# Optimization experiments

Measured on AMD Instinct MI355X. Metric: run time of the kernel, lower is better.

Reference implementation:

```python
import jax, jax.numpy as jnp
import numpy as np

N = 50000      # nodes
E = 200000     # edges
IN = 768       # in_dim
HID = 256      # hidden_dim
OUT = 64       # out_dim
H = 4          # heads in conv1
R = 6          # n_relations
NEG = 0.2      # LeakyReLU negative slope (PyG default)
EPS = 1e-5     # LayerNorm eps


def layer_norm(h, g, b):
    mu = jnp.mean(h, axis=-1, keepdims=True)
    var = jnp.mean((h - mu) ** 2, axis=-1, keepdims=True)
    return (h - mu) * jax.lax.rsqrt(var + EPS) * g + b


def gat_layer(x, src, dst, W, a_src, a_dst, bias, heads, dh):
    # project: [N, heads, dh]
    h = (x @ W).reshape(-1, heads, dh)
    # per-node attention logits [N, heads]
    al_s = jnp.sum(h * a_src, axis=-1)
    al_d = jnp.sum(h * a_dst, axis=-1)
    # per-edge scores (edge j->i: source contributes al_s[j], target al_d[i])
    e = jax.nn.leaky_relu(al_s[src] + al_d[dst], NEG)  # [E, heads]
    # segment softmax over edges sharing the same destination node
    e_max = jax.ops.segment_max(e, dst, num_segments=N)        # [N, heads]
    ex = jnp.exp(e - e_max[dst])                               # [E, heads]
    denom = jax.ops.segment_sum(ex, dst, num_segments=N)       # [N, heads]
    alpha = ex / denom[dst]                                    # [E, heads]
    # weighted scatter-aggregate of source messages
    msg = h[src] * alpha[:, :, None]                            # [E, heads, dh]
    out = jax.ops.segment_sum(msg, dst, num_segments=N)        # [N, heads, dh]
    return out.reshape(-1, heads * dh) + bias


def setup_inputs() -> dict:
    key = jax.random.key(0)
    ks = jax.random.split(key, 16)
    s = 0.05  # keep attention logits tame
    return {
        "x": jax.random.normal(ks[0], (N, IN), jnp.float32),
        "edge_index": jax.random.randint(ks[1], (2, E), 0, N, dtype=jnp.int64),
        "edge_type": jax.random.randint(ks[2], (E,), 0, R, dtype=jnp.int64),
        "edge_emb": jax.random.normal(ks[3], (R, IN), jnp.float32) * s,
        "W1": jax.random.normal(ks[4], (IN, H * (HID // H)), jnp.float32) * s,
        "a_src1": jax.random.normal(ks[5], (H, HID // H), jnp.float32) * s,
        "a_dst1": jax.random.normal(ks[6], (H, HID // H), jnp.float32) * s,
        "b1": jnp.zeros((HID,), jnp.float32),
        "g1": jnp.ones((HID,), jnp.float32),
        "be1": jnp.zeros((HID,), jnp.float32),
        "W2": jax.random.normal(ks[7], (HID, OUT), jnp.float32) * s,
        "a_src2": jax.random.normal(ks[8], (1, OUT), jnp.float32) * s,
        "a_dst2": jax.random.normal(ks[9], (1, OUT), jnp.float32) * s,
        "b2": jnp.zeros((OUT,), jnp.float32),
        "g2": jnp.ones((OUT,), jnp.float32),
        "be2": jnp.zeros((OUT,), jnp.float32),
    }


def reference(x, edge_index, edge_type, edge_emb, W1, a_src1, a_dst1, b1, g1, be1,
              W2, a_src2, a_dst2, b2, g2, be2):
    src, dst = edge_index[0], edge_index[1]
    edge_feat = edge_emb[edge_type]                 # [E, IN]
    x_mod = x.at[src].set(x[src] + edge_feat)
    h = gat_layer(x_mod, src, dst, W1, a_src1, a_dst1, b1, H, HID // H)
    h = layer_norm(h, g1, be1)
    h = jax.nn.elu(h)                                # dropout off (inference)
    h = gat_layer(h, src, dst, W2, a_src2, a_dst2, b2, 1, OUT)
    h = layer_norm(h, g2, be2)
    return h
```

## Files before the change

### kernel.cpp

```cpp
#include <hip/hip_runtime.h>
#include <cstdint>
#include <cstddef>

#define NN 50000
#define NE 200000
#define IND 768
#define HID 256
#define OUTD 64
#define NB 196

typedef __bf16 bf16;
typedef __bf16 bf16x8 __attribute__((ext_vector_type(8)));
typedef float f32x4 __attribute__((ext_vector_type(4)));

__global__ __launch_bounds__(256) void k_edge_prep(const int* __restrict__ ei,
                                                   int* __restrict__ le, int* __restrict__ deg) {
  int e = blockIdx.x * 256 + threadIdx.x;
  if (e < NE) {
    atomicMax(&le[ei[e]], e);
    atomicAdd(&deg[ei[NE + e]], 1);
  }
}

__global__ __launch_bounds__(256) void k_eembz(const float* __restrict__ eemb,
                                               float* __restrict__ ez) {
  int i = blockIdx.x * 256 + threadIdx.x;
  if (i < 7 * IND) ez[i] = (i < 6 * IND) ? eemb[i] : 0.f;
}

__global__ __launch_bounds__(256) void k_prep_a(const float* __restrict__ x,
                                                const int* __restrict__ le,
                                                const int* __restrict__ et,
                                                const float* __restrict__ eembz,
                                                bf16* __restrict__ A1) {
  int idx = blockIdx.x * 256 + threadIdx.x;
  if (idx >= NN * (IND / 8)) return;
  int row = idx / (IND / 8);
  int c = (idx - row * (IND / 8)) * 8;
  int l = le[row];
  int e = (l >= 0) ? et[l] : 6;
  const float* px = x + (size_t)row * IND + c;
  const float* pe = eembz + (size_t)e * IND + c;
  float4 v0 = *(const float4*)px, v1 = *(const float4*)(px + 4);
  float4 e0 = *(const float4*)pe, e1 = *(const float4*)(pe + 4);
  bf16x8 o;
  o[0] = (bf16)(v0.x + e0.x); o[1] = (bf16)(v0.y + e0.y);
  o[2] = (bf16)(v0.z + e0.z); o[3] = (bf16)(v0.w + e0.w);
  o[4] = (bf16)(v1.x + e1.x); o[5] = (bf16)(v1.y + e1.y);
  o[6] = (bf16)(v1.z + e1.z); o[7] = (bf16)(v1.w + e1.w);
  *(bf16x8*)(A1 + (size_t)row * IND + c) = o;
}

__global__ __launch_bounds__(256) void k_scan_block(const int* __restrict__ deg,
                                                    int* __restrict__ excl, int* __restrict__ bsum) {
  __shared__ int sm[256];
  int tid = threadIdx.x;
  int i = blockIdx.x * 256 + tid;
  int v = (i < NN) ? deg[i] : 0;
  sm[tid] = v;
  __syncthreads();
#pragma unroll
  for (int off = 1; off < 256; off <<= 1) {
    int t = (tid >= off) ? sm[tid - off] : 0;
    __syncthreads();
    sm[tid] += t;
    __syncthreads();
  }
  if (i < NN) excl[i] = sm[tid] - v;
  if (tid == 255) bsum[blockIdx.x] = sm[255];
}

__global__ __launch_bounds__(256) void k_scan_partials(const int* __restrict__ bsum,
                                                       int* __restrict__ bbase) {
  __shared__ int sm[256];
  int tid = threadIdx.x;
  int v = (tid < NB) ? bsum[tid] : 0;
  sm[tid] = v;
  __syncthreads();
#pragma unroll
  for (int off = 1; off < 256; off <<= 1) {
    int t = (tid >= off) ? sm[tid - off] : 0;
    __syncthreads();
    sm[tid] += t;
    __syncthreads();
  }
  bbase[tid] = sm[tid] - v;
}

__global__ __launch_bounds__(256) void k_add_base(const int* __restrict__ excl,
                                                  const int* __restrict__ bbase,
                                                  int* __restrict__ rowstart, int* __restrict__ cur) {
  int i = blockIdx.x * 256 + threadIdx.x;
  if (i < NN) {
    int rs = excl[i] + bbase[i >> 8];
    rowstart[i] = rs;
    cur[i] = rs;
  }
}

__global__ __launch_bounds__(256) void k_scatter_csr(const int* __restrict__ ei,
                                                     int* __restrict__ cur, int* __restrict__ csr) {
  int e = blockIdx.x * 256 + threadIdx.x;
  if (e < NE) {
    int d = ei[NE + e];
    int pos = atomicAdd(&cur[d], 1);
    csr[pos] = ei[e];
  }
}

__global__ __launch_bounds__(256) void k_transpose(const float* __restrict__ W,
                                                   bf16* __restrict__ Wt, int K, int NC) {
  int k = blockIdx.x * 256 + threadIdx.x;
  int n = blockIdx.y;
  if (k < K) Wt[n * K + k] = (bf16)W[k * NC + n];
}

__device__ __forceinline__ void gld16(const bf16* g, bf16* l) {
  __builtin_amdgcn_global_load_lds((const __attribute__((address_space(1))) void*)g,
                                   (__attribute__((address_space(3))) void*)l, 16, 0, 0);
}

template <typename OutT>
__global__ __launch_bounds__(256) void k_gemm_bt(const bf16* __restrict__ A,
                                                 const bf16* __restrict__ Bt,
                                                 OutT* __restrict__ C,
                                                 int M, int K, int NC,
                                                 const float* __restrict__ aS,
                                                 const float* __restrict__ aD,
                                                 float* __restrict__ alS,
                                                 float* __restrict__ alD,
                                                 int alStride) {
  __shared__ bf16 As[128 * 32];
  __shared__ bf16 Bs[128 * 32];
  const int tid = threadIdx.x;
  const int lane = tid & 63;
  const int wave = tid >> 6;
  const int wr = wave >> 1, wc = wave & 1;
  const int ln15 = lane & 15, q = lane >> 4;
  const int n0 = blockIdx.x * 128;
  const int m0 = blockIdx.y * 128;

  const int sr = lane >> 2;
  const int scol = (lane & 3) * 8;
  const int gA0 = min(m0 + wave * 32 + sr, M - 1);
  const int gA1 = min(m0 + wave * 32 + 16 + sr, M - 1);
  const int gB0 = min(n0 + wave * 32 + sr, NC - 1);
  const int gB1 = min(n0 + wave * 32 + 16 + sr, NC - 1);
  bf16* lA0 = As + (wave * 32) * 32;
  bf16* lA1 = As + (wave * 32 + 16) * 32;
  bf16* lB0 = Bs + (wave * 32) * 32;
  bf16* lB1 = Bs + (wave * 32 + 16) * 32;

  f32x4 acc[4][4] = {};

  for (int kt = 0; kt < K; kt += 32) {
    gld16(A + (size_t)gA0 * K + kt + scol, lA0);
    gld16(A + (size_t)gA1 * K + kt + scol, lA1);
    gld16(Bt + (size_t)gB0 * K + kt + scol, lB0);
    gld16(Bt + (size_t)gB1 * K + kt + scol, lB1);
    __syncthreads();
    bf16x8 af[4], bfr[4];
#pragma unroll
    for (int i = 0; i < 4; i++)
      af[i] = *(const bf16x8*)(As + (wr * 64 + i * 16 + ln15) * 32 + q * 8);
#pragma unroll
    for (int i = 0; i < 4; i++)
      bfr[i] = *(const bf16x8*)(Bs + (wc * 64 + i * 16 + ln15) * 32 + q * 8);
#pragma unroll
    for (int mi = 0; mi < 4; mi++)
#pragma unroll
      for (int ni = 0; ni < 4; ni++)
        acc[mi][ni] = __builtin_amdgcn_mfma_f32_16x16x32_bf16(af[mi], bfr[ni], acc[mi][ni], 0, 0, 0);
    __syncthreads();
  }

#pragma unroll
  for (int mi = 0; mi < 4; mi++)
#pragma unroll
    for (int ni = 0; ni < 4; ni++)
#pragma unroll
      for (int r = 0; r < 4; r++) {
        int row = m0 + wr * 64 + mi * 16 + q * 4 + r;
        int col = n0 + wc * 64 + ni * 16 + ln15;
        if (row < M && col < NC) C[(size_t)row * NC + col] = (OutT)acc[mi][ni][r];
      }

  if (n0 + wc * 64 < NC) {
    const int hd = (n0 + wc * 64) >> 6;
#pragma unroll
    for (int mi = 0; mi < 4; mi++)
#pragma unroll
      for (int r = 0; r < 4; r++) {
        float ps = 0.f, pd = 0.f;
#pragma unroll
        for (int ni = 0; ni < 4; ni++) {
          int col = n0 + wc * 64 + ni * 16 + ln15;
          float w_s = (col < NC) ? aS[col] : 0.f;
          float w_d = (col < NC) ? aD[col] : 0.f;
          ps += acc[mi][ni][r] * w_s;
          pd += acc[mi][ni][r] * w_d;
        }
#pragma unroll
        for (int off = 1; off < 16; off <<= 1) {
          ps += __shfl_xor(ps, off);
          pd += __shfl_xor(pd, off);
        }
        int row = m0 + wr * 64 + mi * 16 + q * 4 + r;
        if (ln15 == 0 && row < M) {
          alS[row * alStride + hd] = ps;
          alD[row * alStride + hd] = pd;
        }
      }
  }
}

__global__ __launch_bounds__(256) void k_agg_ln1(const int* __restrict__ rowstart,
                                                 const int* __restrict__ deg,
                                                 const int* __restrict__ csr,
                                                 const bf16* __restrict__ h1,
                                                 const float* __restrict__ alS,
                                                 const float* __restrict__ alD,
                                                 const float* __restrict__ b1,
                                                 const float* __restrict__ g1,
                                                 const float* __restrict__ be1,
                                                 bf16* __restrict__ hln) {
  __shared__ float red[8];
  int n = blockIdx.x, f = threadIdx.x, hd = f >> 6;
  int start = rowstart[n], cnt = deg[n];
  float ald = alD[n * 4 + hd];
  float accv = 0.f, accw = 0.f;
  for (int j = 0; j < cnt; j++) {
    int s = csr[start + j];
    float logit = alS[s * 4 + hd] + ald;
    logit = logit >= 0.f ? logit : 0.2f * logit;
    float w = __expf(logit);
    accv += w * (float)h1[(size_t)s * HID + f];
    accw += w;
  }
  float v = (cnt > 0) ? accv / accw : 0.f;
  v += b1[f];
  float s = v, ss = v * v;
#pragma unroll
  for (int off = 32; off; off >>= 1) { s += __shfl_xor(s, off); ss += __shfl_xor(ss, off); }
  if ((f & 63) == 0) { red[f >> 6] = s; red[4 + (f >> 6)] = ss; }
  __syncthreads();
  float tot = red[0] + red[1] + red[2] + red[3];
  float tss = red[4] + red[5] + red[6] + red[7];
  float mu = tot * (1.f / HID);
  float var = tss * (1.f / HID) - mu * mu;
  float y = (v - mu) * rsqrtf(var + 1e-5f) * g1[f] + be1[f];
  y = y > 0.f ? y : __expf(y) - 1.f;
  hln[(size_t)n * HID + f] = (bf16)y;
}

__global__ __launch_bounds__(64) void k_agg_ln2(const int* __restrict__ rowstart,
                                                const int* __restrict__ deg,
                                                const int* __restrict__ csr,
                                                const float* __restrict__ h2,
                                                const float* __restrict__ alS,
                                                const float* __restrict__ alD,
                                                const float* __restrict__ b2,
                                                const float* __restrict__ g2,
                                                const float* __restrict__ be2,
                                                float* __restrict__ out) {
  int n = blockIdx.x, f = threadIdx.x;
  int start = rowstart[n], cnt = deg[n];
  float ald = alD[n];
  float accv = 0.f, accw = 0.f;
  for (int j = 0; j < cnt; j++) {
    int s = csr[start + j];
    float logit = alS[s] + ald;
    logit = logit >= 0.f ? logit : 0.2f * logit;
    float w = __expf(logit);
    accv += w * h2[(size_t)s * OUTD + f];
    accw += w;
  }
  float v = (cnt > 0) ? accv / accw : 0.f;
  v += b2[f];
  float s = v, ss = v * v;
#pragma unroll
  for (int off = 32; off; off >>= 1) { s += __shfl_xor(s, off); ss += __shfl_xor(ss, off); }
  float mu = s * (1.f / OUTD);
  float var = ss * (1.f / OUTD) - mu * mu;
  out[(size_t)n * OUTD + f] = (v - mu) * rsqrtf(var + 1e-5f) * g2[f] + be2[f];
}

extern "C" void kernel_launch(void* const* d_in, const int* in_sizes, int n_in,
                              void* d_out, int out_size, void* d_ws, size_t ws_size,
                              hipStream_t stream) {
  const float* x    = (const float*)d_in[0];
  const int*   ei   = (const int*)d_in[1];
  const int*   et   = (const int*)d_in[2];
  const float* eemb = (const float*)d_in[3];
  const float* W1   = (const float*)d_in[4];
  const float* as1  = (const float*)d_in[5];
  const float* ad1  = (const float*)d_in[6];
  const float* b1   = (const float*)d_in[7];
  const float* g1   = (const float*)d_in[8];
  const float* be1  = (const float*)d_in[9];
  const float* W2   = (const float*)d_in[10];
  const float* as2  = (const float*)d_in[11];
  const float* ad2  = (const float*)d_in[12];
  const float* b2   = (const float*)d_in[13];
  const float* g2   = (const float*)d_in[14];
  const float* be2  = (const float*)d_in[15];
  float* out = (float*)d_out;

  char* base = (char*)d_ws;
  size_t off = 0;
  auto alloc = [&](size_t bytes) -> void* {
    void* p = base + off;
    off = (off + bytes + 255) & ~(size_t)255;
    return p;
  };
  int*   le    = (int*)alloc((size_t)NN * 4);
  int*   deg   = (int*)alloc((size_t)NN * 4);
  int*   excl  = (int*)alloc((size_t)NN * 4);
  int*   bsum  = (int*)alloc(256 * 4);
  int*   bbase = (int*)alloc(256 * 4);
  int*   rowst = (int*)alloc((size_t)NN * 4);
  int*   cur   = (int*)alloc((size_t)NN * 4);
  int*   csr   = (int*)alloc((size_t)NE * 4);
  bf16*  h1    = (bf16*)alloc((size_t)NN * HID * 2);
  float* alS1  = (float*)alloc((size_t)NN * 4 * 4);
  float* alD1  = (float*)alloc((size_t)NN * 4 * 4);
  bf16*  W1t   = (bf16*)alloc((size_t)HID * IND * 2);
  bf16*  W2t   = (bf16*)alloc((size_t)OUTD * HID * 2);
  float* eembz = (float*)alloc((size_t)7 * IND * 4);
  char*  R     = (char*)alloc((size_t)NN * IND * 2);
  bf16*  A1    = (bf16*)R;
  bf16*  hln   = (bf16*)R;
  float* h2    = (float*)(R + (size_t)NN * HID * 2);
  float* alS2  = (float*)(R + (size_t)NN * HID * 2 + (size_t)NN * OUTD * 4);
  float* alD2  = (float*)(R + (size_t)NN * HID * 2 + (size_t)NN * OUTD * 4 + (size_t)NN * 4);

  hipMemsetAsync(le, 0xFF, (size_t)NN * 4, stream);
  hipMemsetAsync(deg, 0, (size_t)NN * 4, stream);

  k_edge_prep<<<(NE + 255) / 256, 256, 0, stream>>>(ei, le, deg);
  k_eembz<<<(7 * IND + 255) / 256, 256, 0, stream>>>(eemb, eembz);
  k_prep_a<<<(NN * (IND / 8) + 255) / 256, 256, 0, stream>>>(x, le, et, eembz, A1);
  k_scan_block<<<NB, 256, 0, stream>>>(deg, excl, bsum);
  k_scan_partials<<<1, 256, 0, stream>>>(bsum, bbase);
  k_add_base<<<NB, 256, 0, stream>>>(excl, bbase, rowst, cur);
  k_scatter_csr<<<(NE + 255) / 256, 256, 0, stream>>>(ei, cur, csr);

  k_transpose<<<dim3(3, HID), 256, 0, stream>>>(W1, W1t, IND, HID);
  k_transpose<<<dim3(1, OUTD), 256, 0, stream>>>(W2, W2t, HID, OUTD);

  k_gemm_bt<bf16><<<dim3(2, (NN + 127) / 128), 256, 0, stream>>>(
      A1, W1t, h1, NN, IND, HID, as1, ad1, alS1, alD1, 4);
  k_agg_ln1<<<NN, 256, 0, stream>>>(rowst, deg, csr, h1, alS1, alD1, b1, g1, be1, hln);

  k_gemm_bt<float><<<dim3(1, (NN + 127) / 128), 256, 0, stream>>>(
      hln, W2t, h2, NN, HID, OUTD, as2, ad2, alS2, alD2, 1);
  k_agg_ln2<<<NN, 64, 0, stream>>>(rowst, deg, csr, h2, alS2, alD2, b2, g2, be2, out);
}
```

Measured before the change: 481.1 us.

## Double-buffer GEMM loads, add 64-wide tile variant, repack aggregation kernels per wave

The GEMM now double-buffers its LDS tiles and issues the next k-slice loads before computing on the current one, using explicit vmcnt waits. A template parameter adds a 64-column tile variant so the second GEMM no longer wastes half of a 128-wide tile. The layer-1 aggregation now processes one node per wave with 4 features per lane, using vectorized bf16 loads and a block-free LayerNorm reduction. Layer-2 aggregation packs 4 nodes into each 256-thread block. The hand-written waitcnt counts must match the number of issued global_load_lds calls, and they add complexity.

```diff
diff --git a/kernel.cpp b/kernel.cpp
--- a/kernel.cpp
+++ b/kernel.cpp
@@ -11,6 +11,7 @@
 
 typedef __bf16 bf16;
 typedef __bf16 bf16x8 __attribute__((ext_vector_type(8)));
+typedef __bf16 bf16x4 __attribute__((ext_vector_type(4)));
 typedef float f32x4 __attribute__((ext_vector_type(4)));
 
 __global__ __launch_bounds__(256) void k_edge_prep(const int* __restrict__ ei,
@@ -120,7 +121,7 @@
                                    (__attribute__((address_space(3))) void*)l, 16, 0, 0);
 }
 
-template <typename OutT>
+template <typename OutT, int TN>
 __global__ __launch_bounds__(256) void k_gemm_bt(const bf16* __restrict__ A,
                                                  const bf16* __restrict__ Bt,
                                                  OutT* __restrict__ C,
@@ -130,57 +131,88 @@
                                                  float* __restrict__ alS,
                                                  float* __restrict__ alD,
                                                  int alStride) {
-  __shared__ bf16 As[128 * 32];
-  __shared__ bf16 Bs[128 * 32];
+  constexpr int MI = (TN == 128) ? 4 : 2;
+  constexpr int WROWS = MI * 16;
+  __shared__ bf16 As[2][128 * 32];
+  __shared__ bf16 Bs[2][TN * 32];
   const int tid = threadIdx.x;
   const int lane = tid & 63;
   const int wave = tid >> 6;
-  const int wr = wave >> 1, wc = wave & 1;
+  const int wr = (TN == 128) ? (wave >> 1) : wave;
+  const int wc = (TN == 128) ? (wave & 1) : 0;
   const int ln15 = lane & 15, q = lane >> 4;
-  const int n0 = blockIdx.x * 128;
+  const int n0 = blockIdx.x * TN;
   const int m0 = blockIdx.y * 128;
 
   const int sr = lane >> 2;
   const int scol = (lane & 3) * 8;
   const int gA0 = min(m0 + wave * 32 + sr, M - 1);
   const int gA1 = min(m0 + wave * 32 + 16 + sr, M - 1);
-  const int gB0 = min(n0 + wave * 32 + sr, NC - 1);
-  const int gB1 = min(n0 + wave * 32 + 16 + sr, NC - 1);
-  bf16* lA0 = As + (wave * 32) * 32;
-  bf16* lA1 = As + (wave * 32 + 16) * 32;
-  bf16* lB0 = Bs + (wave * 32) * 32;
-  bf16* lB1 = Bs + (wave * 32 + 16) * 32;
-
-  f32x4 acc[4][4] = {};
-
-  for (int kt = 0; kt < K; kt += 32) {
-    gld16(A + (size_t)gA0 * K + kt + scol, lA0);
-    gld16(A + (size_t)gA1 * K + kt + scol, lA1);
-    gld16(Bt + (size_t)gB0 * K + kt + scol, lB0);
-    gld16(Bt + (size_t)gB1 * K + kt + scol, lB1);
-    __syncthreads();
-    bf16x8 af[4], bfr[4];
+  int gB0, gB1 = 0;
+  if constexpr (TN == 128) {
+    gB0 = min(n0 + wave * 32 + sr, NC - 1);
+    gB1 = min(n0 + wave * 32 + 16 + sr, NC - 1);
+  } else {
+    gB0 = min(n0 + wave * 16 + sr, NC - 1);
+  }
+
+  auto stage = [&](int buf, int kt) {
+    gld16(A + (size_t)gA0 * K + kt + scol, &As[buf][(wave * 32) * 32]);
+    gld16(A + (size_t)gA1 * K + kt + scol, &As[buf][(wave * 32 + 16) * 32]);
+    if constexpr (TN == 128) {
+      gld16(Bt + (size_t)gB0 * K + kt + scol, &Bs[buf][(wave * 32) * 32]);
+      gld16(Bt + (size_t)gB1 * K + kt + scol, &Bs[buf][(wave * 32 + 16) * 32]);
+    } else {
+      gld16(Bt + (size_t)gB0 * K + kt + scol, &Bs[buf][(wave * 16) * 32]);
+    }
+  };
+
+  f32x4 acc[MI][4] = {};
+
+  auto compute = [&](int buf) {
+    bf16x8 af[MI], bfr[4];
+#pragma unroll
+    for (int i = 0; i < MI; i++)
+      af[i] = *(const bf16x8*)(&As[buf][(wr * WROWS + i * 16 + ln15) * 32 + q * 8]);
 #pragma unroll
     for (int i = 0; i < 4; i++)
-      af[i] = *(const bf16x8*)(As + (wr * 64 + i * 16 + ln15) * 32 + q * 8);
-#pragma unroll
-    for (int i = 0; i < 4; i++)
-      bfr[i] = *(const bf16x8*)(Bs + (wc * 64 + i * 16 + ln15) * 32 + q * 8);
-#pragma unroll
-    for (int mi = 0; mi < 4; mi++)
+      bfr[i] = *(const bf16x8*)(&Bs[buf][(wc * 64 + i * 16 + ln15) * 32 + q * 8]);
+#pragma unroll
+    for (int mi = 0; mi < MI; mi++)
 #pragma unroll
       for (int ni = 0; ni < 4; ni++)
         acc[mi][ni] = __builtin_amdgcn_mfma_f32_16x16x32_bf16(af[mi], bfr[ni], acc[mi][ni], 0, 0, 0);
-    __syncthreads();
-  }
-
-#pragma unroll
-  for (int mi = 0; mi < 4; mi++)
+  };
+
+  const int NT = K >> 5;
+
+  stage(0, 0);
+  stage(1, 32);
+  int cur = 0;
+  for (int t = 0; t < NT; ++t) {
+    if (t < NT - 1) {
+      if constexpr (TN == 128) asm volatile("s_waitcnt vmcnt(4)" ::: "memory");
+      else                     asm volatile("s_waitcnt vmcnt(3)" ::: "memory");
+    } else {
+      asm volatile("s_waitcnt vmcnt(0)" ::: "memory");
+    }
+    __builtin_amdgcn_s_barrier();
+    compute(cur);
+    if (t + 2 < NT) {
+      asm volatile("s_waitcnt lgkmcnt(0)" ::: "memory");
+      __builtin_amdgcn_s_barrier();
+      stage(cur, (t + 2) << 5);
+    }
+    cur ^= 1;
+  }
+
+#pragma unroll
+  for (int mi = 0; mi < MI; mi++)
 #pragma unroll
     for (int ni = 0; ni < 4; ni++)
 #pragma unroll
       for (int r = 0; r < 4; r++) {
-        int row = m0 + wr * 64 + mi * 16 + q * 4 + r;
+        int row = m0 + wr * WROWS + mi * 16 + q * 4 + r;
         int col = n0 + wc * 64 + ni * 16 + ln15;
         if (row < M && col < NC) C[(size_t)row * NC + col] = (OutT)acc[mi][ni][r];
       }
@@ -188,7 +220,7 @@
   if (n0 + wc * 64 < NC) {
     const int hd = (n0 + wc * 64) >> 6;
 #pragma unroll
-    for (int mi = 0; mi < 4; mi++)
+    for (int mi = 0; mi < MI; mi++)
 #pragma unroll
       for (int r = 0; r < 4; r++) {
         float ps = 0.f, pd = 0.f;
@@ -205,7 +237,7 @@
           ps += __shfl_xor(ps, off);
           pd += __shfl_xor(pd, off);
         }
-        int row = m0 + wr * 64 + mi * 16 + q * 4 + r;
+        int row = m0 + wr * WROWS + mi * 16 + q * 4 + r;
         if (ln15 == 0 && row < M) {
           alS[row * alStride + hd] = ps;
           alD[row * alStride + hd] = pd;
@@ -224,46 +256,65 @@
                                                  const float* __restrict__ g1,
                                                  const float* __restrict__ be1,
                                                  bf16* __restrict__ hln) {
-  __shared__ float red[8];
-  int n = blockIdx.x, f = threadIdx.x, hd = f >> 6;
+  const int n = blockIdx.x * 4 + (threadIdx.x >> 6);
+  const int lane = threadIdx.x & 63;
+  const int f0 = lane * 4;
+  const int hd = lane >> 4;
   int start = rowstart[n], cnt = deg[n];
   float ald = alD[n * 4 + hd];
-  float accv = 0.f, accw = 0.f;
+  float accv0 = 0.f, accv1 = 0.f, accv2 = 0.f, accv3 = 0.f, accw = 0.f;
   for (int j = 0; j < cnt; j++) {
     int s = csr[start + j];
     float logit = alS[s * 4 + hd] + ald;
     logit = logit >= 0.f ? logit : 0.2f * logit;
     float w = __expf(logit);
-    accv += w * (float)h1[(size_t)s * HID + f];
+    bf16x4 hv = *(const bf16x4*)(h1 + (size_t)s * HID + f0);
+    accv0 += w * (float)hv[0];
+    accv1 += w * (float)hv[1];
+    accv2 += w * (float)hv[2];
+    accv3 += w * (float)hv[3];
     accw += w;
   }
-  float v = (cnt > 0) ? accv / accw : 0.f;
-  v += b1[f];
-  float s = v, ss = v * v;
+  float inv = (cnt > 0) ? 1.f / accw : 0.f;
+  float4 bv = *(const float4*)(b1 + f0);
+  float v0 = accv0 * inv + bv.x;
+  float v1 = accv1 * inv + bv.y;
+  float v2 = accv2 * inv + bv.z;
+  float v3 = accv3 * inv + bv.w;
+  float s = v0 + v1 + v2 + v3;
+  float ss = v0 * v0 + v1 * v1 + v2 * v2 + v3 * v3;
 #pragma unroll
   for (int off = 32; off; off >>= 1) { s += __shfl_xor(s, off); ss += __shfl_xor(ss, off); }
-  if ((f & 63) == 0) { red[f >> 6] = s; red[4 + (f >> 6)] = ss; }
-  __syncthreads();
-  float tot = red[0] + red[1] + red[2] + red[3];
-  float tss = red[4] + red[5] + red[6] + red[7];
-  float mu = tot * (1.f / HID);
-  float var = tss * (1.f / HID) - mu * mu;
-  float y = (v - mu) * rsqrtf(var + 1e-5f) * g1[f] + be1[f];
-  y = y > 0.f ? y : __expf(y) - 1.f;
-  hln[(size_t)n * HID + f] = (bf16)y;
-}
-
-__global__ __launch_bounds__(64) void k_agg_ln2(const int* __restrict__ rowstart,
-                                                const int* __restrict__ deg,
-                                                const int* __restrict__ csr,
-                                                const float* __restrict__ h2,
-                                                const float* __restrict__ alS,
-                                                const float* __restrict__ alD,
-                                                const float* __restrict__ b2,
-                                                const float* __restrict__ g2,
-                                                const float* __restrict__ be2,
-                                                float* __restrict__ out) {
-  int n = blockIdx.x, f = threadIdx.x;
+  float mu = s * (1.f / HID);
+  float var = ss * (1.f / HID) - mu * mu;
+  float rs = rsqrtf(var + 1e-5f);
+  float4 gv = *(const float4*)(g1 + f0);
+  float4 ev = *(const float4*)(be1 + f0);
+  float y0 = (v0 - mu) * rs * gv.x + ev.x;
+  float y1 = (v1 - mu) * rs * gv.y + ev.y;
+  float y2 = (v2 - mu) * rs * gv.z + ev.z;
+  float y3 = (v3 - mu) * rs * gv.w + ev.w;
+  y0 = y0 > 0.f ? y0 : __expf(y0) - 1.f;
+  y1 = y1 > 0.f ? y1 : __expf(y1) - 1.f;
+  y2 = y2 > 0.f ? y2 : __expf(y2) - 1.f;
+  y3 = y3 > 0.f ? y3 : __expf(y3) - 1.f;
+  bf16x4 o;
+  o[0] = (bf16)y0; o[1] = (bf16)y1; o[2] = (bf16)y2; o[3] = (bf16)y3;
+  *(bf16x4*)(hln + (size_t)n * HID + f0) = o;
+}
+
+__global__ __launch_bounds__(256) void k_agg_ln2(const int* __restrict__ rowstart,
+                                                 const int* __restrict__ deg,
+                                                 const int* __restrict__ csr,
+                                                 const float* __restrict__ h2,
+                                                 const float* __restrict__ alS,
+                                                 const float* __restrict__ alD,
+                                                 const float* __restrict__ b2,
+                                                 const float* __restrict__ g2,
+                                                 const float* __restrict__ be2,
+                                                 float* __restrict__ out) {
+  const int n = blockIdx.x * 4 + (threadIdx.x >> 6);
+  const int f = threadIdx.x & 63;
   int start = rowstart[n], cnt = deg[n];
   float ald = alD[n];
   float accv = 0.f, accw = 0.f;
@@ -348,11 +399,11 @@
   k_transpose<<<dim3(3, HID), 256, 0, stream>>>(W1, W1t, IND, HID);
   k_transpose<<<dim3(1, OUTD), 256, 0, stream>>>(W2, W2t, HID, OUTD);
 
-  k_gemm_bt<bf16><<<dim3(2, (NN + 127) / 128), 256, 0, stream>>>(
+  k_gemm_bt<bf16, 128><<<dim3(2, (NN + 127) / 128), 256, 0, stream>>>(
       A1, W1t, h1, NN, IND, HID, as1, ad1, alS1, alD1, 4);
-  k_agg_ln1<<<NN, 256, 0, stream>>>(rowst, deg, csr, h1, alS1, alD1, b1, g1, be1, hln);
-
-  k_gemm_bt<float><<<dim3(1, (NN + 127) / 128), 256, 0, stream>>>(
+  k_agg_ln1<<<NN / 4, 256, 0, stream>>>(rowst, deg, csr, h1, alS1, alD1, b1, g1, be1, hln);
+
+  k_gemm_bt<float, 64><<<dim3(1, (NN + 127) / 128), 256, 0, stream>>>(
       hln, W2t, h2, NN, HID, OUTD, as2, ad2, alS2, alD2, 1);
-  k_agg_ln2<<<NN, 64, 0, stream>>>(rowst, deg, csr, h2, alS2, alD2, b2, g2, be2, out);
-}
+  k_agg_ln2<<<NN / 4, 256, 0, stream>>>(rowst, deg, csr, h2, alS2, alD2, b2, g2, be2, out);
+}
```

Measured after the change: 438.0 us. 1.1x faster.
